# Performance work log

Measured on AMD Instinct MI355X. Metric: run time of the kernel, lower is better.

The kernel has to match this reference:

```python
import jax, jax.numpy as jnp
import numpy as np

B, S, D, N = 16, 1024, 512, 2048
SPECTRAL_RADIUS = 0.95
SPARSITY = 0.01  # effective_sparsity = max(0.01, 5/N) = 0.01 for N=2048


def setup_inputs() -> dict:
    key = jax.random.key(0)
    k_x, k_fb, k_wraw, k_mask, k_win, k_wfb = jax.random.split(key, 6)
    x_seq = jax.random.normal(k_x, (B, S, D), dtype=jnp.float32)
    feedback_seq = jax.random.normal(k_fb, (B, S, D), dtype=jnp.float32)
    initial_state = jnp.zeros((B, N), dtype=jnp.float32)
    # Fixed random reservoir: sparse gaussian rescaled to spectral radius ~0.95.
    # For an NxN gaussian with density p, spectral radius ~= sqrt(N*p), so we
    # rescale by SPECTRAL_RADIUS / sqrt(N*p) (the torch code uses the exact
    # max eigenvalue; this approximation preserves the same math structure).
    W_raw = jax.random.normal(k_wraw, (N, N), dtype=jnp.float32)
    mask = (jax.random.uniform(k_mask, (N, N)) < SPARSITY).astype(jnp.float32)
    W_res = W_raw * mask * (SPECTRAL_RADIUS / jnp.sqrt(N * SPARSITY))
    W_in = jax.random.normal(k_win, (N, D), dtype=jnp.float32) * 0.1
    W_fb = jax.random.normal(k_wfb, (N, D), dtype=jnp.float32) * 0.1
    return {
        "x_seq": x_seq,
        "feedback_seq": feedback_seq,
        "initial_state": initial_state,
        "W_res": W_res,
        "W_in": W_in,
        "W_fb": W_fb,
    }


def reference(x_seq, feedback_seq, initial_state, W_res, W_in, W_fb):
    # Precompute input + feedback projections as one batched GEMM each
    # (same math as per-step einsums: 'bi,ni->bn' == x @ W.T).
    drive = jnp.einsum("bsd,nd->sbn", x_seq, W_in) + jnp.einsum(
        "bsd,nd->sbn", feedback_seq, W_fb
    )  # (S, B, N)

    def step(state, drive_t):
        # pre = state @ W_res.T + W_in x_t + W_fb fb_t
        new_state = jnp.tanh(state @ W_res.T + drive_t)
        return new_state, new_state

    _, states = jax.lax.scan(step, initial_state, drive)  # (S, B, N)
    return jnp.transpose(states, (1, 0, 2))  # (B, S, N)
```

## Files before the change

### kernel.cpp

```cpp
#include <hip/hip_runtime.h>
#include <stdint.h>

typedef unsigned short u16;
typedef unsigned int   u32;
typedef __attribute__((ext_vector_type(8))) short short8;
typedef __attribute__((ext_vector_type(4))) float f32x4;

#define CAP   52

__device__ __forceinline__ u16 rne_bf16(float f){
  u32 u = __float_as_uint(f);
  u32 r = (u + 0x7fffu + ((u >> 16) & 1u)) >> 16;
  return (u16)r;
}
__device__ __forceinline__ float bf16_to_f(u16 h){
  return __uint_as_float(((u32)h) << 16);
}
__device__ __forceinline__ float tanh_fast(float x){
  float e = __expf(2.0f * x);
  return 1.0f - 2.0f / (e + 1.0f);
}

__global__ __launch_bounds__(256) void pack_a_k(const float* __restrict__ x,
                                                const float* __restrict__ fb,
                                                u16* __restrict__ A){
  int idx = blockIdx.x * 256 + threadIdx.x;
  int m = idx >> 9, d = idx & 511;
  float xv = x[idx];
  float fv = fb[idx];
  u16 xh = rne_bf16(xv); u16 xl = rne_bf16(xv - bf16_to_f(xh));
  u16 fh = rne_bf16(fv); u16 fl = rne_bf16(fv - bf16_to_f(fh));
  size_t base = (size_t)m * 2048;
  A[base + d]        = xh;
  A[base + 512 + d]  = fh;
  A[base + 1024 + d] = xl;
  A[base + 1536 + d] = fl;
}

__global__ __launch_bounds__(256) void pack_b_k(const float* __restrict__ Win,
                                                const float* __restrict__ Wfb,
                                                const int* __restrict__ rowperm,
                                                u16* __restrict__ Bm){
  int idx = blockIdx.x * 256 + threadIdx.x;
  int n = idx >> 9, d = idx & 511;
  int row = rowperm[n];
  float iv = Win[(size_t)row * 512 + d];
  float fv = Wfb[(size_t)row * 512 + d];
  u16 ih = rne_bf16(iv); u16 il = rne_bf16(iv - bf16_to_f(ih));
  u16 fh = rne_bf16(fv); u16 fl = rne_bf16(fv - bf16_to_f(fh));
  size_t base = (size_t)n * 3072;
  Bm[base + d]        = ih;
  Bm[base + 512 + d]  = fh;
  Bm[base + 1024 + d] = ih;
  Bm[base + 1536 + d] = fh;
  Bm[base + 2048 + d] = il;
  Bm[base + 2560 + d] = fl;
}

#define GLDS(gp, lp) __builtin_amdgcn_global_load_lds( \
    (const __attribute__((address_space(1))) void*)(gp), \
    (__attribute__((address_space(3))) void*)(lp), 16, 0, 0)

__global__ __launch_bounds__(256) void gemm_k(const u16* __restrict__ A,
                                              const u16* __restrict__ Bm,
                                              float* __restrict__ C){
  __shared__ __align__(16) u16 As[128 * 32];
  __shared__ __align__(16) u16 Bs[128 * 32];
  const int tid = threadIdx.x;
  const int w = tid >> 6, l = tid & 63;
  const int bid = blockIdx.x;
  const int mt = bid >> 4, nt = bid & 15;
  const int m0 = mt * 128, n0 = nt * 128;
  const int srow = tid >> 2;
  const int scol = (tid & 3) * 8;
  const int wr = w & 1, wc = w >> 1;
  const int lhi = l >> 4, llo = l & 15;

  f32x4 acc[4][4];
  #pragma unroll
  for (int i = 0; i < 4; i++)
    #pragma unroll
    for (int j = 0; j < 4; j++)
      acc[i][j] = (f32x4){0.f, 0.f, 0.f, 0.f};

  for (int kt = 0; kt < 96; ++kt){
    int k = kt * 32;
    int keff = (k >= 2048) ? (k - 2048) : k;
    #pragma unroll
    for (int r = 0; r < 2; r++){
      const u16* ga = A  + (size_t)(m0 + r * 64 + srow) * 2048 + keff + scol;
      GLDS(ga, &As[r * 2048 + w * 512]);
      const u16* gb = Bm + (size_t)(n0 + r * 64 + srow) * 3072 + k + scol;
      GLDS(gb, &Bs[r * 2048 + w * 512]);
    }
    __syncthreads();
    short8 af[4], bf[4];
    #pragma unroll
    for (int i = 0; i < 4; i++){
      af[i] = *(const short8*)&As[(wr * 64 + i * 16 + llo) * 32 + lhi * 8];
      bf[i] = *(const short8*)&Bs[(wc * 64 + i * 16 + llo) * 32 + lhi * 8];
    }
    #pragma unroll
    for (int i = 0; i < 4; i++)
      #pragma unroll
      for (int j = 0; j < 4; j++)
        acc[i][j] = __builtin_amdgcn_mfma_f32_16x16x32_bf16(af[i], bf[j], acc[i][j], 0, 0, 0);
    __syncthreads();
  }
  #pragma unroll
  for (int i = 0; i < 4; i++)
    #pragma unroll
    for (int j = 0; j < 4; j++)
      #pragma unroll
      for (int rg = 0; rg < 4; rg++){
        int mr = m0 + wr * 64 + i * 16 + lhi * 4 + rg;
        int nc = n0 + wc * 64 + j * 16 + llo;
        C[(size_t)mr * 2048 + nc] = acc[i][j][rg];
      }
}

__global__ __launch_bounds__(256) void count_k(const float* __restrict__ W,
                                               int* __restrict__ nnz){
  int gt = blockIdx.x * 256 + threadIdx.x;
  int row = gt >> 6, l = gt & 63;
  const float* wr = W + (size_t)row * 2048;
  int c = 0;
  for (int i = 0; i < 32; i++) c += (wr[i * 64 + l] != 0.0f) ? 1 : 0;
  for (int off = 32; off; off >>= 1) c += __shfl_down(c, off, 64);
  if (l == 0) nnz[row] = c;
}

__global__ __launch_bounds__(1024) void sort_k(const int* __restrict__ nnz,
                                               u32* __restrict__ rowsp,
                                               int* __restrict__ L1a,
                                               int* __restrict__ rowperm){
  __shared__ int hist[64], off[64], cur[64];
  __shared__ int order[2048];
  int tid = threadIdx.x;
  if (tid < 64){ hist[tid] = 0; cur[tid] = 0; }
  __syncthreads();
  for (int r = tid; r < 2048; r += 1024){
    int b = nnz[r]; if (b > 63) b = 63;
    atomicAdd(&hist[b], 1);
  }
  __syncthreads();
  if (tid == 0){
    int run = 0;
    for (int b = 63; b >= 0; b--){ off[b] = run; run += hist[b]; }
  }
  __syncthreads();
  for (int r = tid; r < 2048; r += 1024){
    int b = nnz[r]; if (b > 63) b = 63;
    int pos = off[b] + atomicAdd(&cur[b], 1);
    order[pos] = r;
  }
  __syncthreads();
  int rA = order[tid], rB = order[2047 - tid];
  rowsp[tid] = (u32)rA | ((u32)rB << 16);
  L1a[tid] = nnz[rA];
  rowperm[tid] = rA;
  rowperm[tid + 1024] = rB;
}

__global__ __launch_bounds__(256) void fill_k(const float* __restrict__ W,
                                              const u32* __restrict__ rowsp,
                                              u32* __restrict__ wpk){
  int gt = blockIdx.x * 256 + threadIdx.x;
  int p = gt >> 6, l = gt & 63;
  u32 rp = rowsp[p];
  int rA = (int)(rp & 0xffffu), rB = (int)(rp >> 16);
  int base = 0;
  for (int h = 0; h < 2; h++){
    int row = h ? rB : rA;
    const float* wr = W + (size_t)row * 2048;
    int cnt = 0;
    for (int i = 0; i < 32; i++){
      int c = i * 64 + l;
      float v = wr[c];
      unsigned long long m = __ballot(v != 0.0f);
      int pre = __popcll(m & ((1ull << l) - 1ull));
      if (v != 0.0f){
        int s = base + cnt + pre;
        if (s < CAP){
          u32 u = __float_as_uint(v);
          u = (u + 0x1000u) & 0xFFFFE000u;
          wpk[s * 1024 + p] = u | ((u32)c << 2);
        }
      }
      cnt += __popcll(m);
    }
    base += cnt;
  }
  for (int s = base + l; s < CAP; s += 64)
    wpk[s * 1024 + p] = 0u;
}

__global__ __attribute__((amdgpu_flat_work_group_size(1024, 1024),
                          amdgpu_waves_per_eu(4, 4)))
void rnn_k(float* __restrict__ out,
           const float* __restrict__ init,
           const u32* __restrict__ wpkg,
           const u32* __restrict__ rowsp,
           const int* __restrict__ L1a){
  const int tid = threadIdx.x, b = blockIdx.x;
  u32 wk[CAP];
  #pragma unroll
  for (int k = 0; k < CAP; k++) wk[k] = wpkg[k * 1024 + tid];
  u32 rp = rowsp[tid];
  int rA = (int)(rp & 0xffffu), rB = (int)(rp >> 16);
  int L1 = L1a[tid];

  __shared__ float st[2048];
  st[tid]        = init[(size_t)b * 2048 + tid];
  st[tid + 1024] = init[(size_t)b * 2048 + tid + 1024];
  __syncthreads();
  const char* stb = (const char*)st;

  float* ob = out + (size_t)b * 1024 * 2048;
  float dA = __builtin_nontemporal_load(&ob[tid]);
  float dB = __builtin_nontemporal_load(&ob[tid + 1024]);
  for (int t = 0; t < 1024; t++){
    float* orow = ob + (size_t)t * 2048;
    const float* nrow = ob + (size_t)((t + 1) & 1023) * 2048;
    float dA2 = __builtin_nontemporal_load(&nrow[tid]);
    float dB2 = __builtin_nontemporal_load(&nrow[tid + 1024]);
    float aAll = 0.f, aA = 0.f;
    #pragma unroll
    for (int k = 0; k < CAP; k++){
      u32 w = wk[k];
      float sv = *(const float*)(stb + (w & 0x1FFCu));
      float pv = __uint_as_float(w & 0xFFFFE000u) * sv;
      aAll += pv;
      aA += (k < L1) ? pv : 0.0f;
    }
    float preA = aA + dA;
    float preB = (aAll - aA) + dB;
    __syncthreads();
    float sA = tanh_fast(preA);
    float sB = tanh_fast(preB);
    st[rA] = sA; st[rB] = sB;
    __syncthreads();
    __builtin_nontemporal_store(st[tid], &orow[tid]);
    __builtin_nontemporal_store(st[tid + 1024], &orow[tid + 1024]);
    dA = dA2; dB = dB2;
  }
}

extern "C" void kernel_launch(void* const* d_in, const int* in_sizes, int n_in,
                              void* d_out, int out_size, void* d_ws, size_t ws_size,
                              hipStream_t stream) {
  const float* x    = (const float*)d_in[0];
  const float* fb   = (const float*)d_in[1];
  const float* init = (const float*)d_in[2];
  const float* Wres = (const float*)d_in[3];
  const float* Win  = (const float*)d_in[4];
  const float* Wfb  = (const float*)d_in[5];
  float* out = (float*)d_out;

  char* w8 = (char*)d_ws;
  u16*  A_pack = (u16*)(w8);
  u16*  B_pack = (u16*)(w8 + 67108864);
  u32*  wpk    = (u32*) (w8 + 79691776);
  int*  nnz    = (int*) (w8 + 79904768);
  u32*  rowsp  = (u32*) (w8 + 79912960);
  int*  L1a    = (int*) (w8 + 79917056);
  int*  rowperm= (int*) (w8 + 79921152);

  pack_a_k<<<32768, 256, 0, stream>>>(x, fb, A_pack);
  count_k<<<512, 256, 0, stream>>>(Wres, nnz);
  sort_k<<<1, 1024, 0, stream>>>(nnz, rowsp, L1a, rowperm);
  pack_b_k<<<4096, 256, 0, stream>>>(Win, Wfb, rowperm, B_pack);
  fill_k<<<256, 256, 0, stream>>>(Wres, rowsp, wpk);
  gemm_k<<<2048, 256, 0, stream>>>(A_pack, B_pack, out);
  rnn_k<<<16, 1024, 0, stream>>>(out, init, wpk, rowsp, L1a);
}
```

Before: 3.261 ms.

## Double-buffer reservoir state and reorder sparse slots to avoid LDS bank conflicts

The recurrent kernel now keeps two copies of the state in shared memory and alternates between them each step. This removes one of the two barriers per time step. The packing kernel is rewritten so each thread serially scans its two rows. It then greedily assigns nonzeros to slots so that lanes in a wave hit distinct LDS banks at each slot, and padding slots point at the target bank. The cost is a slower, poorly parallel preprocessing kernel (16x64 threads, each walking 4096 floats) in exchange for fewer bank conflicts and fewer syncs in the 1024-step loop.

```diff
diff --git a/kernel.cpp b/kernel.cpp
--- a/kernel.cpp
+++ b/kernel.cpp
@@ -162,37 +162,53 @@
   rowperm[tid + 1024] = rB;
 }
 
-__global__ __launch_bounds__(256) void fill_k(const float* __restrict__ W,
-                                              const u32* __restrict__ rowsp,
-                                              u32* __restrict__ wpk){
-  int gt = blockIdx.x * 256 + threadIdx.x;
-  int p = gt >> 6, l = gt & 63;
+__global__ __launch_bounds__(64) void fill_k(const float* __restrict__ W,
+                                             const u32* __restrict__ rowsp,
+                                             u32* __restrict__ wpk){
+  int p = blockIdx.x * 64 + threadIdx.x;
   u32 rp = rowsp[p];
   int rA = (int)(rp & 0xffffu), rB = (int)(rp >> 16);
-  int base = 0;
+  u32 itv[64];
+  unsigned char ibk[64];
+  int nA = 0, nT = 0;
   for (int h = 0; h < 2; h++){
-    int row = h ? rB : rA;
-    const float* wr = W + (size_t)row * 2048;
-    int cnt = 0;
-    for (int i = 0; i < 32; i++){
-      int c = i * 64 + l;
+    const float* wr = W + (size_t)(h ? rB : rA) * 2048;
+    for (int c = 0; c < 2048; c++){
       float v = wr[c];
-      unsigned long long m = __ballot(v != 0.0f);
-      int pre = __popcll(m & ((1ull << l) - 1ull));
-      if (v != 0.0f){
-        int s = base + cnt + pre;
-        if (s < CAP){
-          u32 u = __float_as_uint(v);
-          u = (u + 0x1000u) & 0xFFFFE000u;
-          wpk[s * 1024 + p] = u | ((u32)c << 2);
-        }
+      if (v != 0.0f && nT < 64){
+        u32 u = __float_as_uint(v);
+        u = (u + 0x1000u) & 0xFFFFE000u;
+        itv[nT] = u | ((u32)c << 2);
+        ibk[nT] = (unsigned char)(c & 31);
+        nT++;
       }
-      cnt += __popcll(m);
     }
-    base += cnt;
-  }
-  for (int s = base + l; s < CAP; s += 64)
-    wpk[s * 1024 + p] = 0u;
+    if (h == 0) nA = nT;
+  }
+  if (nA > CAP) nA = CAP;
+  if (nT > CAP) nT = CAP;
+  int off = (p & 63) >> 1;
+  unsigned long long used = 0ull;
+  for (int s = 0; s < CAP; s++){
+    int tgt = (off + s) & 31;
+    u32 word;
+    if (s >= nT){
+      word = (u32)tgt << 2;
+    } else {
+      int lo = (s < nA) ? 0 : nA;
+      int hi = (s < nA) ? nA : nT;
+      int best = lo, bd = 99;
+      for (int i = lo; i < hi; i++){
+        if (used & (1ull << i)) continue;
+        int d = (ibk[i] - tgt) & 31;
+        if (d > 16) d = 32 - d;
+        if (d < bd){ bd = d; best = i; if (d == 0) break; }
+      }
+      used |= 1ull << best;
+      word = itv[best];
+    }
+    wpk[s * 1024 + p] = word;
+  }
 }
 
 __global__ __attribute__((amdgpu_flat_work_group_size(1024, 1024),
@@ -203,47 +219,60 @@
            const u32* __restrict__ rowsp,
            const int* __restrict__ L1a){
   const int tid = threadIdx.x, b = blockIdx.x;
-  u32 wk[CAP];
+  u32 wv[CAP], ad[CAP];
   #pragma unroll
-  for (int k = 0; k < CAP; k++) wk[k] = wpkg[k * 1024 + tid];
+  for (int k = 0; k < CAP; k++){
+    u32 w = wpkg[k * 1024 + tid];
+    wv[k] = w & 0xFFFFE000u;
+    ad[k] = w & 0x1FFCu;
+  }
   u32 rp = rowsp[tid];
-  int rA = (int)(rp & 0xffffu), rB = (int)(rp >> 16);
-  int L1 = L1a[tid];
-
-  __shared__ float st[2048];
+  const int rA4 = (int)(rp & 0xffffu) << 2;
+  const int rB4 = (int)(rp >> 16) << 2;
+  const int L1 = L1a[tid];
+
+  __shared__ float st[4096];
   st[tid]        = init[(size_t)b * 2048 + tid];
   st[tid + 1024] = init[(size_t)b * 2048 + tid + 1024];
   __syncthreads();
   const char* stb = (const char*)st;
+  char* stw = (char*)st;
+  const int t4a = tid << 2, t4b = (tid + 1024) << 2;
 
   float* ob = out + (size_t)b * 1024 * 2048;
   float dA = __builtin_nontemporal_load(&ob[tid]);
   float dB = __builtin_nontemporal_load(&ob[tid + 1024]);
-  for (int t = 0; t < 1024; t++){
-    float* orow = ob + (size_t)t * 2048;
-    const float* nrow = ob + (size_t)((t + 1) & 1023) * 2048;
-    float dA2 = __builtin_nontemporal_load(&nrow[tid]);
-    float dB2 = __builtin_nontemporal_load(&nrow[tid + 1024]);
-    float aAll = 0.f, aA = 0.f;
-    #pragma unroll
-    for (int k = 0; k < CAP; k++){
-      u32 w = wk[k];
-      float sv = *(const float*)(stb + (w & 0x1FFCu));
-      float pv = __uint_as_float(w & 0xFFFFE000u) * sv;
-      aAll += pv;
-      aA += (k < L1) ? pv : 0.0f;
-    }
-    float preA = aA + dA;
-    float preB = (aAll - aA) + dB;
-    __syncthreads();
-    float sA = tanh_fast(preA);
-    float sB = tanh_fast(preB);
-    st[rA] = sA; st[rB] = sB;
-    __syncthreads();
-    __builtin_nontemporal_store(st[tid], &orow[tid]);
-    __builtin_nontemporal_store(st[tid + 1024], &orow[tid + 1024]);
-    dA = dA2; dB = dB2;
-  }
+
+#define ESN_STEP(T, RDOFF, WROFF) { \
+    float* orow = ob + (size_t)(T) * 2048; \
+    const float* nrow = ob + (size_t)(((T) + 1) & 1023) * 2048; \
+    float dA2 = __builtin_nontemporal_load(&nrow[tid]); \
+    float dB2 = __builtin_nontemporal_load(&nrow[tid + 1024]); \
+    float aAll = 0.f, aA = 0.f; \
+    _Pragma("unroll") \
+    for (int k = 0; k < CAP; k++){ \
+      float sv = *(const float*)(stb + (RDOFF) + ad[k]); \
+      float pv = __uint_as_float(wv[k]) * sv; \
+      aAll += pv; \
+      aA   += (k < L1) ? pv : 0.0f; \
+    } \
+    float preA = aA + dA; \
+    float preB = (aAll - aA) + dB; \
+    float sA = tanh_fast(preA); \
+    float sB = tanh_fast(preB); \
+    *(float*)(stw + (WROFF) + rA4) = sA; \
+    *(float*)(stw + (WROFF) + rB4) = sB; \
+    __syncthreads(); \
+    __builtin_nontemporal_store(*(const float*)(stb + (WROFF) + t4a), &orow[tid]); \
+    __builtin_nontemporal_store(*(const float*)(stb + (WROFF) + t4b), &orow[tid + 1024]); \
+    dA = dA2; dB = dB2; \
+  }
+
+  for (int t = 0; t < 1024; t += 2){
+    ESN_STEP(t, 0, 8192)
+    ESN_STEP(t + 1, 8192, 0)
+  }
+#undef ESN_STEP
 }
 
 extern "C" void kernel_launch(void* const* d_in, const int* in_sizes, int n_in,
@@ -270,7 +299,7 @@
   count_k<<<512, 256, 0, stream>>>(Wres, nnz);
   sort_k<<<1, 1024, 0, stream>>>(nnz, rowsp, L1a, rowperm);
   pack_b_k<<<4096, 256, 0, stream>>>(Win, Wfb, rowperm, B_pack);
-  fill_k<<<256, 256, 0, stream>>>(Wres, rowsp, wpk);
+  fill_k<<<16, 64, 0, stream>>>(Wres, rowsp, wpk);
   gemm_k<<<2048, 256, 0, stream>>>(A_pack, B_pack, out);
   rnn_k<<<16, 1024, 0, stream>>>(out, init, wpk, rowsp, L1a);
 }
```

New measurement: 5.872 ms. +80.1%, slower.

## Schedule sparse weight slots to avoid LDS bank conflicts; drop mask in inner loop

Applied to the files above, without the earlier changes.

Adds a preprocessing kernel that reorders each thread's packed nonzero entries so that, for each slot index, the 64 lanes of a wave spread their shared-memory state reads across the 32 LDS banks with bounded conflicts. Padding slots are pointed at under-used banks instead of address zero. The packed weight encoding is changed so the embedded address bits are part of the rounded float value, which lets the recurrent inner loop use the word directly as a float and skip one AND per term. The cost is a small serial greedy scheduling kernel in setup and slightly perturbed low mantissa bits of the weights.

```diff
diff --git a/kernel.cpp b/kernel.cpp
--- a/kernel.cpp
+++ b/kernel.cpp
@@ -182,9 +182,10 @@
       if (v != 0.0f){
         int s = base + cnt + pre;
         if (s < CAP){
+          u32 addr = (u32)c << 2;
           u32 u = __float_as_uint(v);
-          u = (u + 0x1000u) & 0xFFFFE000u;
-          wpk[s * 1024 + p] = u | ((u32)c << 2);
+          u = ((u - addr + 0x1000u) & 0xFFFFE000u) + addr;
+          wpk[s * 1024 + p] = u;
         }
       }
       cnt += __popcll(m);
@@ -193,6 +194,56 @@
   }
   for (int s = base + l; s < CAP; s += 64)
     wpk[s * 1024 + p] = 0u;
+}
+
+__global__ __launch_bounds__(64) void sched_k(u32* wpk,
+                                              const u32* __restrict__ rowsp,
+                                              const int* __restrict__ nnz){
+  __shared__ u32 itm[64 * CAP];
+  __shared__ int cnt[32];
+  const int lane = threadIdx.x;
+  const int p = blockIdx.x * 64 + lane;
+  u32 rp = rowsp[p];
+  int rA = (int)(rp & 0xffffu), rB = (int)(rp >> 16);
+  int L1 = nnz[rA]; if (L1 > CAP) L1 = CAP;
+  int nT = L1 + nnz[rB]; if (nT > CAP) nT = CAP;
+  for (int k = 0; k < CAP; k++) itm[lane * CAP + k] = wpk[k * 1024 + p];
+  __syncthreads();
+  unsigned long long used = 0ull;
+  for (int s = 0; s < CAP; s++){
+    if (lane < 32) cnt[lane] = 0;
+    __syncthreads();
+    u32 word;
+    if (s < nT){
+      int lo = (s < L1) ? 0 : L1;
+      int hi = (s < L1) ? L1 : nT;
+      int chosen = -1;
+      for (int capc = 2; chosen < 0; capc++){
+        for (int j = lo; j < hi; j++){
+          if (used & (1ull << j)) continue;
+          u32 w = itm[lane * CAP + j];
+          int bk = (int)((w >> 2) & 31u);
+          int old = atomicAdd(&cnt[bk], 1);
+          if (old < capc){ chosen = j; break; }
+          atomicSub(&cnt[bk], 1);
+        }
+      }
+      used |= 1ull << chosen;
+      word = itm[lane * CAP + chosen];
+    } else {
+      int bsel = -1;
+      for (int capc = 2; bsel < 0; capc++){
+        for (int bk = 0; bk < 32; bk++){
+          int old = atomicAdd(&cnt[bk], 1);
+          if (old < capc){ bsel = bk; break; }
+          atomicSub(&cnt[bk], 1);
+        }
+      }
+      word = (u32)bsel << 2;
+    }
+    __syncthreads();
+    wpk[s * 1024 + p] = word;
+  }
 }
 
 __global__ __attribute__((amdgpu_flat_work_group_size(1024, 1024),
@@ -229,7 +280,7 @@
     for (int k = 0; k < CAP; k++){
       u32 w = wk[k];
       float sv = *(const float*)(stb + (w & 0x1FFCu));
-      float pv = __uint_as_float(w & 0xFFFFE000u) * sv;
+      float pv = __uint_as_float(w) * sv;
       aAll += pv;
       aA += (k < L1) ? pv : 0.0f;
     }
@@ -271,6 +322,7 @@
   sort_k<<<1, 1024, 0, stream>>>(nnz, rowsp, L1a, rowperm);
   pack_b_k<<<4096, 256, 0, stream>>>(Win, Wfb, rowperm, B_pack);
   fill_k<<<256, 256, 0, stream>>>(Wres, rowsp, wpk);
+  sched_k<<<16, 64, 0, stream>>>(wpk, rowsp, nnz);
   gemm_k<<<2048, 256, 0, stream>>>(A_pack, B_pack, out);
   rnn_k<<<16, 1024, 0, stream>>>(out, init, wpk, rowsp, L1a);
 }
```

Measured after the change: 3.162 ms. -3.0%, faster.
